# Optimization experiments

Measured on AMD Instinct MI355X. Metric: run time of the kernel, lower is better.

## Reference

```python
import jax, jax.numpy as jnp
import numpy as np

N, E, L, H, C, F, NCLASS, NGRAPH = 50000, 800000, 3, 2, 64, 128, 10, 64
NEG_SLOPE = 0.2


def setup_inputs() -> dict:
    key = jax.random.key(0)
    ks = jax.random.split(key, 8)
    x = jax.random.normal(ks[0], (N, F), dtype=jnp.float32)
    edge_index = jax.random.randint(ks[1], (2, E), 0, N, dtype=jnp.int64)
    batch = jnp.sort(jax.random.randint(ks[2], (N,), 0, NGRAPH, dtype=jnp.int64))
    s = 1.0 / np.sqrt(F)
    W = jax.random.normal(ks[3], (L, F, H * C), dtype=jnp.float32) * s
    att_src = jax.random.normal(ks[4], (L, H, C), dtype=jnp.float32) * s
    att_dst = jax.random.normal(ks[5], (L, H, C), dtype=jnp.float32) * s
    bias = jnp.zeros((L, H * C), dtype=jnp.float32)
    lin_w = jax.random.normal(ks[6], (H * C, NCLASS), dtype=jnp.float32) * s
    lin_b = jnp.zeros((NCLASS,), dtype=jnp.float32)
    return {"x": x, "edge_index": edge_index, "batch": batch, "W": W,
            "att_src": att_src, "att_dst": att_dst, "bias": bias,
            "lin_w": lin_w, "lin_b": lin_b}


def _gat_layer(x, src, dst, w, a_s, a_d, b):
    n = x.shape[0]
    h = (x @ w).reshape(n, H, C)                      # [N,H,C]
    alpha_src = jnp.sum(h * a_s, axis=-1)             # [N,H]
    alpha_dst = jnp.sum(h * a_d, axis=-1)             # [N,H]
    e = jax.nn.leaky_relu(alpha_src[src] + alpha_dst[dst], NEG_SLOPE)  # [E2,H]
    # scatter-softmax over incoming edges of each destination node
    m = jax.ops.segment_max(e, dst, num_segments=n)
    p = jnp.exp(e - m[dst])
    z = jax.ops.segment_sum(p, dst, num_segments=n)
    alpha = p / z[dst]                                # [E2,H]
    msg = h[src] * alpha[:, :, None]                  # [E2,H,C]
    out = jax.ops.segment_sum(msg, dst, num_segments=n)  # [N,H,C]
    return out.reshape(n, H * C) + b


def reference(x, edge_index, batch, W, att_src, att_dst, bias, lin_w, lin_b):
    n = x.shape[0]
    # PyG GATConv default: add self-loops
    loop = jnp.arange(n, dtype=edge_index.dtype)
    src = jnp.concatenate([edge_index[0], loop])
    dst = jnp.concatenate([edge_index[1], loop])
    for l in range(L):
        x = _gat_layer(x, src, dst, W[l], att_src[l], att_dst[l], bias[l])
        x = jax.nn.elu(x)  # activation; dropout/bn inactive (eval, use_bn=False)
    # global mean pool per graph
    sums = jax.ops.segment_sum(x, batch, num_segments=NGRAPH)
    cnt = jax.ops.segment_sum(jnp.ones((n,), x.dtype), batch, num_segments=NGRAPH)
    pooled = sums / jnp.maximum(cnt, 1.0)[:, None]    # [NGRAPH, H*C]
    logits = pooled @ lin_w + lin_b
    return jax.nn.softmax(logits, axis=1)
```

## Files before the change

### kernel.cpp

```cpp
#include <hip/hip_runtime.h>
#include <math.h>

#define NNODES 50000
#define NEDGES 800000
#define NLAYERS 3
#define NHEADS 2
#define NCH 64
#define FDIM 128
#define NCLS 10
#define NGRAPH 64
#define NEG_SLOPE 0.2f
#define GEMMB ((NNODES + 127) / 128)
#define NB 391
#define RADB 391
#define PCH 8

#define WAVE_SYNC()                      \
  do {                                   \
    __builtin_amdgcn_wave_barrier();     \
    __asm__ volatile("" ::: "memory");   \
  } while (0)

typedef __attribute__((ext_vector_type(8))) short bf16x8;
typedef __attribute__((ext_vector_type(4))) float f32x4;

__device__ __forceinline__ unsigned short f2bf(float f) {
  unsigned int u = __builtin_bit_cast(unsigned int, f);
  unsigned int r = u + 0x7FFFu + ((u >> 16) & 1u);
  return (unsigned short)(r >> 16);
}
__device__ __forceinline__ float bflo(unsigned v) {
  return __builtin_bit_cast(float, v << 16);
}
__device__ __forceinline__ float bfhi(unsigned v) {
  return __builtin_bit_cast(float, v & 0xFFFF0000u);
}

__global__ __launch_bounds__(256) void k_wprep(const float* __restrict__ W,
                                               unsigned* __restrict__ Wt,
                                               const int* __restrict__ batch,
                                               int* __restrict__ goff,
                                               float* __restrict__ gsum,
                                               int* __restrict__ bcnt,
                                               int* __restrict__ done) {
  __shared__ float Lt[128][132];
  int l = blockIdx.x;
  int t = threadIdx.x;
  if (l == NLAYERS) {
    if (t < NGRAPH) {
      int lo = 0, hi = NNODES;
      while (lo < hi) {
        int mid = (lo + hi) >> 1;
        if (batch[mid] < t) lo = mid + 1;
        else hi = mid;
      }
      goff[t] = lo;
    }
    if (t == 0) {
      goff[NGRAPH] = NNODES;
      *done = 0;
    }
    for (int i = t; i < NGRAPH * FDIM; i += 256) gsum[i] = 0.f;
    for (int i = t; i < NB; i += 256) bcnt[i] = 0;
    return;
  }
  const float* Wl = W + (size_t)l * FDIM * FDIM;
  unsigned* Wtl = Wt + (size_t)l * FDIM * FDIM / 2;
#pragma unroll
  for (int i = 0; i < 16; ++i) {
    int k = (t >> 5) + 8 * i;
    int n4 = (t & 31) * 4;
    float4 v = *(const float4*)(Wl + (size_t)k * 128 + n4);
    Lt[k][n4 + 0] = v.x;
    Lt[k][n4 + 1] = v.y;
    Lt[k][n4 + 2] = v.z;
    Lt[k][n4 + 3] = v.w;
  }
  __syncthreads();
  int n = t >> 1;
  int kh = (t & 1) * 64;
  for (int kk = 0; kk < 64; kk += 2) {
    unsigned pk = (unsigned)f2bf(Lt[kh + kk][n]) |
                  ((unsigned)f2bf(Lt[kh + kk + 1][n]) << 16);
    Wtl[n * 64 + (kh >> 1) + (kk >> 1)] = pk;
  }
}

template <bool BF16IN>
__device__ __forceinline__ void gemm_body(int blk, const void* __restrict__ Xv,
                                          const unsigned* __restrict__ Wt,
                                          const float* __restrict__ a_sL,
                                          const float* __restrict__ a_dL,
                                          unsigned* __restrict__ Hb,
                                          float* __restrict__ as_,
                                          float* __restrict__ ad_) {
  int t = threadIdx.x;
  int lane = t & 63;
  int w = t >> 6;
  int n16 = lane & 15;
  int quad = lane >> 4;
  int rowb = blk * 128 + w * 32;

  size_t rb[2];
  rb[0] = (size_t)min(rowb + n16, NNODES - 1) * 128;
  rb[1] = (size_t)min(rowb + 16 + n16, NNODES - 1) * 128;

  f32x4 acc[2][8];
#pragma unroll
  for (int mt = 0; mt < 2; ++mt)
#pragma unroll
    for (int nt = 0; nt < 8; ++nt) {
      f32x4 z = {0.f, 0.f, 0.f, 0.f};
      acc[mt][nt] = z;
    }
#pragma unroll
  for (int kk = 0; kk < 4; ++kk) {
    bf16x8 af[2];
#pragma unroll
    for (int mt = 0; mt < 2; ++mt) {
      if constexpr (BF16IN) {
        const unsigned short* xp = (const unsigned short*)Xv + rb[mt];
        af[mt] = *(const bf16x8*)(xp + kk * 32 + quad * 8);
      } else {
        const float* xp = (const float*)Xv + rb[mt];
        float4 va = *(const float4*)(xp + kk * 32 + quad * 8);
        float4 vb = *(const float4*)(xp + kk * 32 + quad * 8 + 4);
        af[mt][0] = (short)f2bf(va.x); af[mt][1] = (short)f2bf(va.y);
        af[mt][2] = (short)f2bf(va.z); af[mt][3] = (short)f2bf(va.w);
        af[mt][4] = (short)f2bf(vb.x); af[mt][5] = (short)f2bf(vb.y);
        af[mt][6] = (short)f2bf(vb.z); af[mt][7] = (short)f2bf(vb.w);
      }
    }
#pragma unroll
    for (int nt = 0; nt < 8; ++nt) {
      bf16x8 bf = *(const bf16x8*)(Wt + (size_t)(nt * 16 + n16) * 64 +
                                   kk * 16 + quad * 4);
      acc[0][nt] =
          __builtin_amdgcn_mfma_f32_16x16x32_bf16(af[0], bf, acc[0][nt], 0, 0, 0);
      acc[1][nt] =
          __builtin_amdgcn_mfma_f32_16x16x32_bf16(af[1], bf, acc[1][nt], 0, 0, 0);
    }
  }

  float asv[8], adv[8];
#pragma unroll
  for (int nt = 0; nt < 8; ++nt) {
    asv[nt] = a_sL[nt * 16 + n16];
    adv[nt] = a_dL[nt * 16 + n16];
  }
#pragma unroll
  for (int mt = 0; mt < 2; ++mt) {
#pragma unroll
    for (int r = 0; r < 4; ++r) {
      int row = rowb + mt * 16 + quad * 4 + r;
      bool ok = (row < NNODES);
      float ps0 = 0.f, pd0 = 0.f, ps1 = 0.f, pd1 = 0.f;
#pragma unroll
      for (int nt = 0; nt < 4; ++nt) {
        ps0 += acc[mt][nt][r] * asv[nt];
        pd0 += acc[mt][nt][r] * adv[nt];
        ps1 += acc[mt][nt + 4][r] * asv[nt + 4];
        pd1 += acc[mt][nt + 4][r] * adv[nt + 4];
      }
#pragma unroll
      for (int off = 1; off < 16; off <<= 1) {
        ps0 += __shfl_xor(ps0, off, 64);
        pd0 += __shfl_xor(pd0, off, 64);
        ps1 += __shfl_xor(ps1, off, 64);
        pd1 += __shfl_xor(pd1, off, 64);
      }
      if (ok && n16 == 0) {
        as_[row * 2 + 0] = ps0;
        as_[row * 2 + 1] = ps1;
        ad_[row * 2 + 0] = pd0;
        ad_[row * 2 + 1] = pd1;
      }
      if (ok) {
#pragma unroll
        for (int nt = 0; nt < 4; ++nt) {
          unsigned pk = (unsigned)f2bf(acc[mt][nt][r]) |
                        ((unsigned)f2bf(acc[mt][nt + 4][r]) << 16);
          Hb[(size_t)row * 64 + nt * 16 + n16] = pk;
        }
      }
    }
  }
}

__global__ __launch_bounds__(256) void k_gemm(
    const unsigned short* __restrict__ Xh, const unsigned* __restrict__ Wt,
    const float* __restrict__ a_sL, const float* __restrict__ a_dL,
    unsigned* __restrict__ Hb, float* __restrict__ as_,
    float* __restrict__ ad_) {
  gemm_body<true>(blockIdx.x, Xh, Wt, a_sL, a_dL, Hb, as_, ad_);
}

__global__ __launch_bounds__(256) void k_front(
    const float* __restrict__ X, const unsigned* __restrict__ Wt,
    const float* __restrict__ a_sL, const float* __restrict__ a_dL,
    unsigned* __restrict__ Hb, float* __restrict__ as_,
    float* __restrict__ ad_, const int* __restrict__ ei, int* __restrict__ bh,
    int* __restrict__ bcnt) {
  int b = blockIdx.x;
  if (b < GEMMB) {
    gemm_body<false>(b, X, Wt, a_sL, a_dL, Hb, as_, ad_);
  } else {
    __shared__ int hist[NB];
    int blk = b - GEMMB;
    int t = threadIdx.x;
    for (int i = t; i < NB; i += 256) hist[i] = 0;
    __syncthreads();
    int e0 = blk * 2048;
#pragma unroll
    for (int i = 0; i < 8; ++i) {
      int e = e0 + i * 256 + t;
      if (e < NEDGES) atomicAdd(&hist[ei[NEDGES + e] >> 7], 1);
    }
    __syncthreads();
    for (int i = t; i < NB; i += 256) {
      int c = hist[i];
      int base = c ? atomicAdd(&bcnt[i], c) : 0;
      bh[i * RADB + blk] = base;
    }
  }
}

__global__ __launch_bounds__(256) void k_passB(const int* __restrict__ ei,
                                               const int* __restrict__ bcnt,
                                               const int* __restrict__ bh,
                                               unsigned* __restrict__ ebuf,
                                               int* __restrict__ bstart) {
  __shared__ int curs[NB];
  __shared__ int ps[256];
  int blk = blockIdx.x, t = threadIdx.x;
  int x0 = (2 * t < NB) ? bcnt[2 * t] : 0;
  int x1 = (2 * t + 1 < NB) ? bcnt[2 * t + 1] : 0;
  int pair = x0 + x1;
  ps[t] = pair;
  __syncthreads();
  for (int off = 1; off < 256; off <<= 1) {
    int v = (t >= off) ? ps[t - off] : 0;
    __syncthreads();
    ps[t] += v;
    __syncthreads();
  }
  int ex = ps[t] - pair;
  if (2 * t < NB) {
    curs[2 * t] = ex + bh[(2 * t) * RADB + blk];
    if (blk == 0) bstart[2 * t] = ex;
  }
  if (2 * t + 1 < NB) {
    curs[2 * t + 1] = ex + x0 + bh[(2 * t + 1) * RADB + blk];
    if (blk == 0) bstart[2 * t + 1] = ex + x0;
  }
  if (blk == 0 && t == 0) bstart[NB] = NEDGES;
  __syncthreads();
  int e0 = blk * 2048;
#pragma unroll
  for (int i = 0; i < 8; ++i) {
    int e = e0 + i * 256 + t;
    if (e < NEDGES) {
      int s = ei[e];
      int d = ei[NEDGES + e];
      int pos = atomicAdd(&curs[d >> 7], 1);
      ebuf[pos] = ((unsigned)s << 7) | (unsigned)(d & 127);
    }
  }
}

__global__ __launch_bounds__(256) void k_passC(const unsigned* __restrict__ ebuf,
                                               const int* __restrict__ bstart,
                                               int* __restrict__ row_ptr,
                                               int* __restrict__ csr) {
  __shared__ int deg[128];
  __shared__ int scn[128];
  int b = blockIdx.x, t = threadIdx.x;
  int node0 = b * 128;
  int nn = min(128, NNODES - node0);
  int estart = bstart[b];
  int eend = bstart[b + 1];
  if (t < 128) deg[t] = 0;
  __syncthreads();
  for (int e = estart + t; e < eend; e += 256)
    atomicAdd(&deg[ebuf[e] & 127], 1);
  __syncthreads();
  if (t < 128) scn[t] = (t < nn) ? deg[t] + 1 : 0;
  __syncthreads();
  for (int off = 1; off < 128; off <<= 1) {
    int v = (t < 128 && t >= off) ? scn[t - off] : 0;
    __syncthreads();
    if (t < 128) scn[t] += v;
    __syncthreads();
  }
  int base = estart + node0;
  if (t < nn) {
    int st = base + (t ? scn[t - 1] : 0);
    row_ptr[node0 + t] = st;
    csr[st] = node0 + t;
    deg[t] = st + 1;
  }
  if (b == 0 && t == 0) row_ptr[NNODES] = NEDGES + NNODES;
  __syncthreads();
  for (int e = estart + t; e < eend; e += 256) {
    unsigned v = ebuf[e];
    int pos = atomicAdd(&deg[v & 127], 1);
    csr[pos] = (int)(v >> 7);
  }
}

__global__ __launch_bounds__(256) void k_aggregate(
    const unsigned* __restrict__ Hb, const float* __restrict__ as_,
    const float* __restrict__ ad_, const int* __restrict__ row_ptr,
    const int* __restrict__ csr, const float* __restrict__ bias,
    float* __restrict__ Xout, unsigned short* __restrict__ XoutH) {
  __shared__ float2 wb[4][64];
  __shared__ int sb[4][64];
  int wv = threadIdx.x >> 6;
  int lane = threadIdx.x & 63;
  int node = blockIdx.x * 4 + wv;
  if (node >= NNODES) return;
  int rs = row_ptr[node], re = row_ptr[node + 1];
  float2 adv = *(const float2*)&ad_[node * 2];
  const unsigned* Hl = Hb + lane;

  float z0 = 0.f, z1 = 0.f, acc0 = 0.f, acc1 = 0.f;
  for (int base = rs; base < re; base += 64) {
    int j = base + lane;
    int s = 0;
    if (j < re) s = csr[j];
    sb[wv][lane] = s;
    WAVE_SYNC();
    unsigned va[8];
#pragma unroll
    for (int u = 0; u < 8; ++u) va[u] = Hl[(size_t)sb[wv][u] * 64];
    float p0 = 0.f, p1 = 0.f;
    if (j < re) {
      float2 asv = *(const float2*)&as_[s * 2];
      float e0 = asv.x + adv.x; e0 = (e0 > 0.f) ? e0 : NEG_SLOPE * e0;
      float e1 = asv.y + adv.y; e1 = (e1 > 0.f) ? e1 : NEG_SLOPE * e1;
      p0 = __expf(e0);
      p1 = __expf(e1);
    }
    z0 += p0;
    z1 += p1;
    wb[wv][lane] = make_float2(p0, p1);
    WAVE_SYNC();
    int cl = min(64, re - base);
    int cl8 = (cl + 7) & ~7;
    int jj = 8;
    for (; jj < cl8; jj += 8) {
      unsigned vb2[8];
#pragma unroll
      for (int u = 0; u < 8; ++u) vb2[u] = Hl[(size_t)sb[wv][jj + u] * 64];
#pragma unroll
      for (int u = 0; u < 8; ++u) {
        float2 w = wb[wv][jj - 8 + u];
        acc0 += w.x * bflo(va[u]);
        acc1 += w.y * bfhi(va[u]);
      }
#pragma unroll
      for (int u = 0; u < 8; ++u) va[u] = vb2[u];
    }
#pragma unroll
    for (int u = 0; u < 8; ++u) {
      float2 w = wb[wv][jj - 8 + u];
      acc0 += w.x * bflo(va[u]);
      acc1 += w.y * bfhi(va[u]);
    }
    WAVE_SYNC();
  }
#pragma unroll
  for (int off = 32; off > 0; off >>= 1) {
    z0 += __shfl_xor(z0, off, 64);
    z1 += __shfl_xor(z1, off, 64);
  }
  float o0 = acc0 / z0 + bias[lane];
  float o1 = acc1 / z1 + bias[64 + lane];
  o0 = (o0 > 0.f) ? o0 : expm1f(o0);
  o1 = (o1 > 0.f) ? o1 : expm1f(o1);
  if (XoutH) {
    XoutH[(size_t)node * 128 + lane] = f2bf(o0);
    XoutH[(size_t)node * 128 + 64 + lane] = f2bf(o1);
  } else {
    Xout[(size_t)node * 128 + lane] = o0;
    Xout[(size_t)node * 128 + 64 + lane] = o1;
  }
}

__global__ __launch_bounds__(256) void k_pool2(const float* __restrict__ Xf,
                                               const int* __restrict__ goff,
                                               float* __restrict__ gsum,
                                               int* __restrict__ done,
                                               const float* __restrict__ lw,
                                               const float* __restrict__ lb,
                                               float* __restrict__ out) {
  __shared__ float red[128];
  __shared__ int lastflag;
  int b = blockIdx.x;
  int g = b >> 3, ch = b & 7;
  int t = threadIdx.x;
  int c = t & 127, rh = t >> 7;
  int s = goff[g], e = goff[g + 1];
  int len = e - s;
  int c0 = s + (len * ch) / PCH;
  int c1 = s + (len * (ch + 1)) / PCH;
  float acc = 0.f;
  for (int n = c0 + rh; n < c1; n += 2) acc += Xf[(size_t)n * 128 + c];
  if (rh) red[c] = acc;
  __syncthreads();
  if (!rh) atomicAdd(&gsum[g * FDIM + c], acc + red[c]);
  __syncthreads();
  if (t == 0) {
    __threadfence();
    int prev = atomicAdd(done, 1);
    lastflag = (prev == NGRAPH * PCH - 1) ? 1 : 0;
  }
  __syncthreads();
  if (!lastflag) return;
  __threadfence();
  if (t < NGRAPH) {
    int g2 = t;
    float cnt = (float)(goff[g2 + 1] - goff[g2]);
    float inv = 1.f / fmaxf(cnt, 1.f);
    float lg[NCLS];
#pragma unroll
    for (int k = 0; k < NCLS; ++k) lg[k] = lb[k];
    for (int cc = 0; cc < FDIM; ++cc) {
      float pv = gsum[g2 * FDIM + cc] * inv;
#pragma unroll
      for (int k = 0; k < NCLS; ++k) lg[k] += pv * lw[cc * NCLS + k];
    }
    float mx = lg[0];
#pragma unroll
    for (int k = 1; k < NCLS; ++k) mx = fmaxf(mx, lg[k]);
    float ssum = 0.f;
#pragma unroll
    for (int k = 0; k < NCLS; ++k) {
      lg[k] = expf(lg[k] - mx);
      ssum += lg[k];
    }
    float invs = 1.f / ssum;
#pragma unroll
    for (int k = 0; k < NCLS; ++k) out[g2 * NCLS + k] = lg[k] * invs;
  }
}


extern "C" void kernel_launch(void* const* d_in, const int* in_sizes, int n_in,
                              void* d_out, int out_size, void* d_ws,
                              size_t ws_size, hipStream_t stream) {
  const float* x = (const float*)d_in[0];
  const int* ei = (const int*)d_in[1];
  const int* batch = (const int*)d_in[2];
  const float* W = (const float*)d_in[3];
  const float* a_s = (const float*)d_in[4];
  const float* a_d = (const float*)d_in[5];
  const float* bias = (const float*)d_in[6];
  const float* lw = (const float*)d_in[7];
  const float* lb = (const float*)d_in[8];
  float* out = (float*)d_out;

  unsigned* Hb = (unsigned*)d_ws;
  float* xb = (float*)(Hb + (size_t)NNODES * 64);
  float* as_ = xb + (size_t)NNODES * 128;
  float* ad_ = as_ + (size_t)NNODES * 2;
  float* gsum = ad_ + (size_t)NNODES * 2;
  int* goff = (int*)(gsum + NGRAPH * FDIM);
  int* bcnt = goff + (NGRAPH + 1);
  int* bstart = bcnt + NB;
  int* row_ptr = bstart + (NB + 1);
  int* csr = row_ptr + (NNODES + 1);
  int* bh = csr + (NEDGES + NNODES);
  unsigned* ebuf = (unsigned*)(bh + NB * RADB);
  unsigned* Wt = ebuf + (NEDGES + 1024);
  unsigned short* xbh = (unsigned short*)(Wt + 3 * 8192);
  int* done = (int*)(xbh + (size_t)NNODES * 128);

  k_wprep<<<NLAYERS + 1, 256, 0, stream>>>(W, Wt, batch, goff, gsum, bcnt,
                                           done);
  k_front<<<GEMMB + RADB, 256, 0, stream>>>(x, Wt, a_s, a_d, Hb, as_, ad_, ei,
                                            bh, bcnt);
  k_passB<<<RADB, 256, 0, stream>>>(ei, bcnt, bh, ebuf, bstart);
  k_passC<<<NB, 256, 0, stream>>>(ebuf, bstart, row_ptr, csr);

  for (int l = 0; l < NLAYERS; ++l) {
    if (l > 0) {
      k_gemm<<<GEMMB, 256, 0, stream>>>(xbh, Wt + (size_t)l * FDIM * FDIM / 2,
                                        a_s + l * FDIM, a_d + l * FDIM, Hb,
                                        as_, ad_);
    }
    unsigned short* oh = (l < NLAYERS - 1) ? xbh : nullptr;
    k_aggregate<<<(NNODES + 3) / 4, 256, 0, stream>>>(
        Hb, as_, ad_, row_ptr, csr, bias + l * FDIM, xb, oh);
  }
  k_pool2<<<NGRAPH * PCH, 256, 0, stream>>>(xb, goff, gsum, done, lw, lb, out);
}
```

Measured before the change: 299.9 us.

## Fuse mean-pool accumulation into last aggregate layer, drop separate pool kernel

The last aggregation layer now reduces each block's four node outputs per graph in shared memory and atomically adds them into per-graph sums, instead of writing the full float feature matrix and re-reading it in a pooling kernel. A small single-block kernel then does the mean, linear layer and softmax, with the sums staged in shared memory. This removes a 25 MB write and read plus the completion-counter logic, at the cost of many more global atomics on a small gsum array and a block-wide barrier in the last layer. The node bounds guard is removed, which depends on NNODES being divisible by 4.

Result: faster. 287.8 us, median of 2 (-4.1%).

```diff
diff --git a/kernel.cpp b/kernel.cpp
--- a/kernel.cpp
+++ b/kernel.cpp
@@ -13,7 +13,6 @@
 #define GEMMB ((NNODES + 127) / 128)
 #define NB 391
 #define RADB 391
-#define PCH 8
 
 #define WAVE_SYNC()                      \
   do {                                   \
@@ -41,8 +40,7 @@
                                                const int* __restrict__ batch,
                                                int* __restrict__ goff,
                                                float* __restrict__ gsum,
-                                               int* __restrict__ bcnt,
-                                               int* __restrict__ done) {
+                                               int* __restrict__ bcnt) {
   __shared__ float Lt[128][132];
   int l = blockIdx.x;
   int t = threadIdx.x;
@@ -56,10 +54,7 @@
       }
       goff[t] = lo;
     }
-    if (t == 0) {
-      goff[NGRAPH] = NNODES;
-      *done = 0;
-    }
+    if (t == 0) goff[NGRAPH] = NNODES;
     for (int i = t; i < NGRAPH * FDIM; i += 256) gsum[i] = 0.f;
     for (int i = t; i < NB; i += 256) bcnt[i] = 0;
     return;
@@ -312,13 +307,15 @@
     const unsigned* __restrict__ Hb, const float* __restrict__ as_,
     const float* __restrict__ ad_, const int* __restrict__ row_ptr,
     const int* __restrict__ csr, const float* __restrict__ bias,
-    float* __restrict__ Xout, unsigned short* __restrict__ XoutH) {
+    unsigned short* __restrict__ XoutH, const int* __restrict__ batchp,
+    float* __restrict__ gsum) {
   __shared__ float2 wb[4][64];
   __shared__ int sb[4][64];
+  __shared__ float outv[4][128];
+  __shared__ int gsl[4];
   int wv = threadIdx.x >> 6;
   int lane = threadIdx.x & 63;
   int node = blockIdx.x * 4 + wv;
-  if (node >= NNODES) return;
   int rs = row_ptr[node], re = row_ptr[node + 1];
   float2 adv = *(const float2*)&ad_[node * 2];
   const unsigned* Hl = Hb + lane;
@@ -382,42 +379,39 @@
     XoutH[(size_t)node * 128 + lane] = f2bf(o0);
     XoutH[(size_t)node * 128 + 64 + lane] = f2bf(o1);
   } else {
-    Xout[(size_t)node * 128 + lane] = o0;
-    Xout[(size_t)node * 128 + 64 + lane] = o1;
-  }
-}
-
-__global__ __launch_bounds__(256) void k_pool2(const float* __restrict__ Xf,
+    outv[wv][lane] = o0;
+    outv[wv][64 + lane] = o1;
+    if (lane == 0) gsl[wv] = batchp[node];
+    __syncthreads();
+    if (threadIdx.x < 128) {
+      int c = threadIdx.x;
+      float acc = outv[0][c];
+      int gcur = gsl[0];
+#pragma unroll
+      for (int w2 = 1; w2 < 4; ++w2) {
+        if (gsl[w2] == gcur) {
+          acc += outv[w2][c];
+        } else {
+          atomicAdd(&gsum[gcur * FDIM + c], acc);
+          gcur = gsl[w2];
+          acc = outv[w2][c];
+        }
+      }
+      atomicAdd(&gsum[gcur * FDIM + c], acc);
+    }
+  }
+}
+
+__global__ __launch_bounds__(256) void k_final(const float* __restrict__ gsum,
                                                const int* __restrict__ goff,
-                                               float* __restrict__ gsum,
-                                               int* __restrict__ done,
                                                const float* __restrict__ lw,
                                                const float* __restrict__ lb,
                                                float* __restrict__ out) {
-  __shared__ float red[128];
-  __shared__ int lastflag;
-  int b = blockIdx.x;
-  int g = b >> 3, ch = b & 7;
+  __shared__ float sg[NGRAPH * 132];
   int t = threadIdx.x;
-  int c = t & 127, rh = t >> 7;
-  int s = goff[g], e = goff[g + 1];
-  int len = e - s;
-  int c0 = s + (len * ch) / PCH;
-  int c1 = s + (len * (ch + 1)) / PCH;
-  float acc = 0.f;
-  for (int n = c0 + rh; n < c1; n += 2) acc += Xf[(size_t)n * 128 + c];
-  if (rh) red[c] = acc;
-  __syncthreads();
-  if (!rh) atomicAdd(&gsum[g * FDIM + c], acc + red[c]);
-  __syncthreads();
-  if (t == 0) {
-    __threadfence();
-    int prev = atomicAdd(done, 1);
-    lastflag = (prev == NGRAPH * PCH - 1) ? 1 : 0;
-  }
-  __syncthreads();
-  if (!lastflag) return;
-  __threadfence();
+  for (int i = t; i < NGRAPH * FDIM; i += 256)
+    sg[(i >> 7) * 132 + (i & 127)] = gsum[i];
+  __syncthreads();
   if (t < NGRAPH) {
     int g2 = t;
     float cnt = (float)(goff[g2 + 1] - goff[g2]);
@@ -426,7 +420,7 @@
 #pragma unroll
     for (int k = 0; k < NCLS; ++k) lg[k] = lb[k];
     for (int cc = 0; cc < FDIM; ++cc) {
-      float pv = gsum[g2 * FDIM + cc] * inv;
+      float pv = sg[g2 * 132 + cc] * inv;
 #pragma unroll
       for (int k = 0; k < NCLS; ++k) lg[k] += pv * lw[cc * NCLS + k];
     }
@@ -474,10 +468,8 @@
   unsigned* ebuf = (unsigned*)(bh + NB * RADB);
   unsigned* Wt = ebuf + (NEDGES + 1024);
   unsigned short* xbh = (unsigned short*)(Wt + 3 * 8192);
-  int* done = (int*)(xbh + (size_t)NNODES * 128);
-
-  k_wprep<<<NLAYERS + 1, 256, 0, stream>>>(W, Wt, batch, goff, gsum, bcnt,
-                                           done);
+
+  k_wprep<<<NLAYERS + 1, 256, 0, stream>>>(W, Wt, batch, goff, gsum, bcnt);
   k_front<<<GEMMB + RADB, 256, 0, stream>>>(x, Wt, a_s, a_d, Hb, as_, ad_, ei,
                                             bh, bcnt);
   k_passB<<<RADB, 256, 0, stream>>>(ei, bcnt, bh, ebuf, bstart);
@@ -490,8 +482,9 @@
                                         as_, ad_);
     }
     unsigned short* oh = (l < NLAYERS - 1) ? xbh : nullptr;
-    k_aggregate<<<(NNODES + 3) / 4, 256, 0, stream>>>(
-        Hb, as_, ad_, row_ptr, csr, bias + l * FDIM, xb, oh);
-  }
-  k_pool2<<<NGRAPH * PCH, 256, 0, stream>>>(xb, goff, gsum, done, lw, lb, out);
-}
+    const int* bp = (l == NLAYERS - 1) ? batch : nullptr;
+    k_aggregate<<<NNODES / 4, 256, 0, stream>>>(Hb, as_, ad_, row_ptr, csr,
+                                                bias + l * FDIM, oh, bp, gsum);
+  }
+  k_final<<<1, 256, 0, stream>>>(gsum, goff, lw, lb, out);
+}
```
